# Kernel optimization log

Measured on AMD Instinct MI355X. Metric: run time of the kernel, lower is better.

Reference implementation:

```python
import jax, jax.numpy as jnp
import numpy as np

N, E, D = 50000, 640000, 128


def setup_inputs() -> dict:
    key = jax.random.key(0)
    ks = jax.random.split(key, 10)
    scale = (2.0 / (D + D)) ** 0.5  # xavier-ish scale for square weights

    def w(k):
        return jax.random.normal(k, (D, D), jnp.float32) * scale

    return {
        "x": jax.random.normal(ks[0], (N, D), jnp.float32),
        "view2": jax.random.normal(ks[1], (N, D), jnp.float32),
        "W_neigh1": w(ks[2]),
        "W_self1": w(ks[3]),
        "b_self1": jnp.zeros((D,), jnp.float32),
        "W_neigh2": w(ks[4]),
        "W_self2": w(ks[5]),
        "b_self2": jnp.zeros((D,), jnp.float32),
        "W_attn": w(ks[6]),
        "b_attn": jnp.zeros((D,), jnp.float32),
        "att": jax.random.normal(ks[7], (1, D), jnp.float32) * 0.1,
        "src": jax.random.randint(ks[8], (E,), 0, N),
        "dst": jax.random.randint(ks[9], (E,), 0, N),
    }


def _sage_mean(h, src, dst, W_neigh, W_self, b_self, n):
    """DGL SAGEConv, aggregator_type='mean', in_feats==out_feats (lin after mp)."""
    msgs = h[src]  # gather: [E, D]
    s = jax.ops.segment_sum(msgs, dst, num_segments=n)  # scatter-add: [N, D]
    deg = jax.ops.segment_sum(jnp.ones((src.shape[0],), h.dtype), dst, num_segments=n)
    h_neigh = jnp.where(deg[:, None] > 0, s / jnp.maximum(deg, 1.0)[:, None], 0.0)
    # rst = fc_self(h_self) + fc_neigh(h_neigh)
    return h @ W_self.T + b_self + h_neigh @ W_neigh.T


def reference(x, view2, W_neigh1, W_self1, b_self1, W_neigh2, W_self2, b_self2,
              W_attn, b_attn, att, src, dst):
    n = x.shape[0]
    # SAGENet: outs = [h, l1(h)/1, l2(l1(h))/2]; res = sum(outs)
    h1 = _sage_mean(x, src, dst, W_neigh1, W_self1, b_self1, n)
    h2 = _sage_mean(h1, src, dst, W_neigh2, W_self2, b_self2, n)
    res = x + h1 + h2 * 0.5
    # Attn semantic fusion over embedding views [res, view2]
    embeds = (res, view2)
    scores = jnp.stack(
        [att[0] @ jnp.tanh(e @ W_attn.T + b_attn).mean(axis=0) for e in embeds]
    )  # [2]
    beta = jax.nn.softmax(scores)
    return beta[0] * res + beta[1] * view2
```

## Files before the change

kernel.cpp:

```cpp
#include <hip/hip_runtime.h>

#define DD 128

using bf16 = __bf16;
typedef __bf16 bf16x8 __attribute__((ext_vector_type(8)));
typedef float f32x4 __attribute__((ext_vector_type(4)));

__device__ inline bf16x8 cvt8(const float* p) {
  f32x4 v0 = *(const f32x4*)p;
  f32x4 v1 = *(const f32x4*)(p + 4);
  bf16x8 r;
  r[0] = (bf16)v0[0]; r[1] = (bf16)v0[1]; r[2] = (bf16)v0[2]; r[3] = (bf16)v0[3];
  r[4] = (bf16)v1[0]; r[5] = (bf16)v1[1]; r[6] = (bf16)v1[2]; r[7] = (bf16)v1[3];
  return r;
}

__device__ inline float ftanh(float x) {
  float e2 = __expf(2.0f * x);
  return 1.0f - 2.0f * __builtin_amdgcn_rcpf(e2 + 1.0f);
}

__device__ inline int swz(int o) { return o ^ (((o >> 8) & 7) << 4); }

__global__ void k_prep(int* __restrict__ cnt, int N,
                       const float* __restrict__ w0, const float* __restrict__ w1,
                       const float* __restrict__ w2, const float* __restrict__ w3,
                       const float* __restrict__ w4, bf16* __restrict__ wb, int totalW,
                       const float* __restrict__ x, bf16* __restrict__ xb, int total8,
                       int nbZ, int nbW) {
  int b = blockIdx.x;
  if (b < nbZ) {
    int i = b * 256 + threadIdx.x;
    if (i < N) cnt[i] = 0;
  } else if (b < nbZ + nbW) {
    int i = (b - nbZ) * 256 + threadIdx.x;
    if (i < totalW) {
      int m = i >> 14;
      int r = i & 16383;
      const float* s = m == 0 ? w0 : m == 1 ? w1 : m == 2 ? w2 : m == 3 ? w3 : w4;
      wb[i] = (bf16)s[r];
    }
  } else {
    int i = (b - nbZ - nbW) * 256 + threadIdx.x;
    if (i < total8) *(bf16x8*)(xb + (size_t)i * 8) = cvt8(x + (size_t)i * 8);
  }
}

__global__ void k_hist(const int* __restrict__ dst, int* __restrict__ cnt, int E) {
  int e = blockIdx.x * 256 + threadIdx.x;
  if (e < E) atomicAdd(&cnt[dst[e]], 1);
}

__global__ __launch_bounds__(256) void k_scan1(const int* __restrict__ cnt,
                                               int* __restrict__ bsum, int N) {
  __shared__ int sm[256];
  int t = threadIdx.x;
  int i = blockIdx.x * 256 + t;
  sm[t] = (i < N) ? cnt[i] : 0;
  __syncthreads();
#pragma unroll
  for (int d = 128; d > 0; d >>= 1) {
    if (t < d) sm[t] += sm[t + d];
    __syncthreads();
  }
  if (t == 0) bsum[blockIdx.x] = sm[0];
}

__global__ __launch_bounds__(256) void k_scan2(int* __restrict__ bsum, int nb) {
  __shared__ int sm[256];
  int t = threadIdx.x;
  int v = (t < nb) ? bsum[t] : 0;
  sm[t] = v;
  __syncthreads();
#pragma unroll
  for (int d = 1; d < 256; d <<= 1) {
    int u = (t >= d) ? sm[t - d] : 0;
    __syncthreads();
    sm[t] += u;
    __syncthreads();
  }
  if (t < nb) bsum[t] = sm[t] - v;
}

__global__ __launch_bounds__(256) void k_scan3(const int* __restrict__ cnt,
                                               const int* __restrict__ bsum,
                                               int* __restrict__ offs,
                                               int* __restrict__ cursor, int N) {
  __shared__ int sm[256];
  int t = threadIdx.x;
  int i = blockIdx.x * 256 + t;
  int v = (i < N) ? cnt[i] : 0;
  sm[t] = v;
  __syncthreads();
#pragma unroll
  for (int d = 1; d < 256; d <<= 1) {
    int u = (t >= d) ? sm[t - d] : 0;
    __syncthreads();
    sm[t] += u;
    __syncthreads();
  }
  int incl = sm[t];
  int base = bsum[blockIdx.x];
  if (i < N) {
    int ex = base + incl - v;
    offs[i] = ex;
    cursor[i] = ex;
    if (i == N - 1) offs[N] = base + incl;
  }
}

__global__ void k_scatter(const int* __restrict__ src, const int* __restrict__ dst,
                          int* __restrict__ cursor, int* __restrict__ ssrc, int E) {
  int e = blockIdx.x * 256 + threadIdx.x;
  if (e < E) {
    int d = dst[e];
    int p = atomicAdd(&cursor[d], 1);
    ssrc[p] = src[e];
  }
}

template <int MODE>
__global__ __launch_bounds__(1024, 1) void k_layer(const bf16* __restrict__ Hb,
                                                   const int* __restrict__ offs,
                                                   const int* __restrict__ ssrc,
                                                   const bf16* __restrict__ Wsb,
                                                   const bf16* __restrict__ Wnb,
                                                   const float* __restrict__ bias,
                                                   const float* __restrict__ Xres,
                                                   bf16* __restrict__ H1out,
                                                   float* __restrict__ Out, int N) {
  __shared__ char smem[65536];
  int t = threadIdx.x;
#pragma unroll
  for (int m = 0; m < 2; ++m) {
    const bf16* wsrc = m ? Wnb : Wsb;
#pragma unroll
    for (int it = 0; it < 2; ++it) {
      int o = (it * 1024 + t) * 16;
      *(bf16x8*)(smem + m * 32768 + swz(o)) = *(const bf16x8*)(wsrc + o / 2);
    }
  }
  __syncthreads();

  int wv = t >> 6;
  int lane = t & 63;
  int tile = blockIdx.x * 16 + wv;
  int n0 = tile << 4;
  if (n0 >= N) return;
  int lr = lane & 15;
  int g = lane >> 4;
  int lk = g << 3;

  const bf16* a1p = Hb + (size_t)(n0 + lr) * DD + lk;
  bf16x8 a1[4];
#pragma unroll
  for (int kk = 0; kk < 4; ++kk) a1[kk] = *(const bf16x8*)(a1p + kk * 32);

  int node = n0 + lr;
  int beg = offs[node], end = offs[node + 1];
  float acc[4][8];
#pragma unroll
  for (int kk = 0; kk < 4; ++kk)
#pragma unroll
    for (int j = 0; j < 8; ++j) acc[kk][j] = 0.f;
  for (int i = beg; i < end; ++i) {
    int s = ssrc[i];
    const bf16* hp = Hb + (size_t)s * DD + lk;
#pragma unroll
    for (int kk = 0; kk < 4; ++kk) {
      bf16x8 v = *(const bf16x8*)(hp + kk * 32);
#pragma unroll
      for (int j = 0; j < 8; ++j) acc[kk][j] += (float)v[j];
    }
  }
  float inv = (end > beg) ? 1.0f / (float)(end - beg) : 0.f;
  bf16x8 a2[4];
#pragma unroll
  for (int kk = 0; kk < 4; ++kk)
#pragma unroll
    for (int j = 0; j < 8; ++j) a2[kk][j] = (bf16)(acc[kk][j] * inv);

  int rb = n0 + (g << 2);
#pragma unroll
  for (int j = 0; j < 8; ++j) {
    int row = j * 16 + lr;
    int rbase = row * 256 + lk * 2;
    f32x4 cs = {0.f, 0.f, 0.f, 0.f};
    f32x4 cn = {0.f, 0.f, 0.f, 0.f};
#pragma unroll
    for (int kk = 0; kk < 4; ++kk) {
      int ro = swz(rbase + kk * 64);
      bf16x8 bs = *(const bf16x8*)(smem + ro);
      bf16x8 bn = *(const bf16x8*)(smem + 32768 + ro);
      cs = __builtin_amdgcn_mfma_f32_16x16x32_bf16(a1[kk], bs, cs, 0, 0, 0);
      cn = __builtin_amdgcn_mfma_f32_16x16x32_bf16(a2[kk], bn, cn, 0, 0, 0);
    }
    int col = j * 16 + lr;
    float bb = bias[col];
#pragma unroll
    for (int r = 0; r < 4; ++r) {
      size_t idx = (size_t)(rb + r) * DD + col;
      float v = cs[r] + cn[r] + bb;
      if (MODE == 0) H1out[idx] = (bf16)v;
      else           Out[idx] = Xres[idx] + (float)Hb[idx] + 0.5f * v;
    }
  }
}

__global__ __launch_bounds__(512, 4) void k_attn2(const float* __restrict__ res,
                                                  const float* __restrict__ v2f,
                                                  const bf16* __restrict__ Wab,
                                                  const float* __restrict__ bias,
                                                  const float* __restrict__ att,
                                                  float* __restrict__ partial,
                                                  int nbA, int N) {
  __shared__ char smem[32768];
  __shared__ float smr[8];
  int t = threadIdx.x;
#pragma unroll
  for (int it = 0; it < 4; ++it) {
    int o = (it * 512 + t) * 16;
    *(bf16x8*)(smem + swz(o)) = *(const bf16x8*)(Wab + o / 2);
  }
  __syncthreads();

  int wv = t >> 6;
  int lane = t & 63;
  int gwid = blockIdx.x * 8 + wv;
  int view = gwid & 1;
  int tile = gwid >> 1;
  int n0 = tile << 4;
  float part = 0.f;
  if (n0 < N) {
    const float* Ef = view ? v2f : res;
    int lr = lane & 15;
    int lk = (lane >> 4) << 3;
    const float* ap = Ef + (size_t)(n0 + lr) * DD + lk;
    bf16x8 a[4];
#pragma unroll
    for (int kk = 0; kk < 4; ++kk) a[kk] = cvt8(ap + kk * 32);
#pragma unroll
    for (int j = 0; j < 8; ++j) {
      int row = j * 16 + lr;
      int rbase = row * 256 + lk * 2;
      f32x4 c = {0.f, 0.f, 0.f, 0.f};
#pragma unroll
      for (int kk = 0; kk < 4; ++kk) {
        bf16x8 bw = *(const bf16x8*)(smem + swz(rbase + kk * 64));
        c = __builtin_amdgcn_mfma_f32_16x16x32_bf16(a[kk], bw, c, 0, 0, 0);
      }
      int col = j * 16 + lr;
      float aw = att[col], bb = bias[col];
#pragma unroll
      for (int r = 0; r < 4; ++r) part += aw * ftanh(c[r] + bb);
    }
  }
#pragma unroll
  for (int d = 1; d < 64; d <<= 1) part += __shfl_xor(part, d);
  if (lane == 0) smr[wv] = part;
  __syncthreads();
  if (t == 0) {
    partial[blockIdx.x]       = smr[0] + smr[2] + smr[4] + smr[6];
    partial[nbA + blockIdx.x] = smr[1] + smr[3] + smr[5] + smr[7];
  }
}

__global__ __launch_bounds__(256) void k_score(const float* __restrict__ partial,
                                               float* __restrict__ scores, int nbA) {
  __shared__ float sm[256];
  int t = threadIdx.x;
#pragma unroll
  for (int v = 0; v < 2; ++v) {
    float s = 0.f;
    for (int i = t; i < nbA; i += 256) s += partial[v * nbA + i];
    sm[t] = s;
    __syncthreads();
#pragma unroll
    for (int d = 128; d > 0; d >>= 1) {
      if (t < d) sm[t] += sm[t + d];
      __syncthreads();
    }
    if (t == 0) scores[v] = sm[0];
    __syncthreads();
  }
}

__global__ void k_fin(float* out, const float* __restrict__ v2,
                      const float* __restrict__ scores, float invN, int total4) {
  int i = blockIdx.x * 256 + threadIdx.x;
  if (i >= total4) return;
  float s0 = scores[0] * invN, s1 = scores[1] * invN;
  float m = fmaxf(s0, s1);
  float e0 = expf(s0 - m), e1 = expf(s1 - m);
  float inv = 1.0f / (e0 + e1);
  float b0 = e0 * inv, b1 = e1 * inv;
  f32x4 r = ((const f32x4*)out)[i];
  f32x4 w = ((const f32x4*)v2)[i];
  f32x4 o;
  o[0] = b0 * r[0] + b1 * w[0];
  o[1] = b0 * r[1] + b1 * w[1];
  o[2] = b0 * r[2] + b1 * w[2];
  o[3] = b0 * r[3] + b1 * w[3];
  ((f32x4*)out)[i] = o;
}

extern "C" void kernel_launch(void* const* d_in, const int* in_sizes, int n_in,
                              void* d_out, int out_size, void* d_ws, size_t ws_size,
                              hipStream_t stream) {
  const float* x   = (const float*)d_in[0];
  const float* v2  = (const float*)d_in[1];
  const float* Wn1 = (const float*)d_in[2];
  const float* Ws1 = (const float*)d_in[3];
  const float* b1  = (const float*)d_in[4];
  const float* Wn2 = (const float*)d_in[5];
  const float* Ws2 = (const float*)d_in[6];
  const float* b2  = (const float*)d_in[7];
  const float* Wa  = (const float*)d_in[8];
  const float* ba  = (const float*)d_in[9];
  const float* att = (const float*)d_in[10];
  const int*  src  = (const int*)d_in[11];
  const int*  dst  = (const int*)d_in[12];
  const int D = in_sizes[4];
  const int N = in_sizes[0] / D;
  const int E = in_sizes[11];
  float* out = (float*)d_out;

  char* ws = (char*)d_ws;
  size_t o = 0;
  auto alloc = [&](size_t bytes) -> void* {
    void* p = ws + o;
    o += (bytes + 255) & ~(size_t)255;
    return p;
  };
  int*  cnt    = (int*)alloc((size_t)N * 4);
  int*  offs   = (int*)alloc((size_t)(N + 1) * 4);
  int*  cursor = (int*)alloc((size_t)N * 4);
  int*  ssrc   = (int*)alloc((size_t)E * 4);
  bf16* xb     = (bf16*)alloc((size_t)N * D * 2);
  bf16* h1b    = (bf16*)alloc((size_t)N * D * 2);
  bf16* wb     = (bf16*)alloc((size_t)5 * D * D * 2);
  float* sc    = (float*)alloc(2 * 4);
  int nb = (N + 255) / 256;
  int*  bsum   = (int*)alloc((size_t)nb * 4);

  int tilesPerView = (N + 15) / 16;
  int attnWaves = 2 * tilesPerView;
  int nbA = (attnWaves + 7) / 8;
  float* apart = (float*)alloc((size_t)2 * nbA * 4);

  int nbZ = (N + 255) / 256;
  int nbW = (5 * D * D + 255) / 256;
  int nbX = (N * D / 8 + 255) / 256;
  k_prep<<<nbZ + nbW + nbX, 256, 0, stream>>>(cnt, N, Ws1, Wn1, Ws2, Wn2, Wa, wb,
                                              5 * D * D, x, xb, N * D / 8, nbZ, nbW);

  k_hist<<<(E + 255) / 256, 256, 0, stream>>>(dst, cnt, E);
  k_scan1<<<nb, 256, 0, stream>>>(cnt, bsum, N);
  k_scan2<<<1, 256, 0, stream>>>(bsum, nb);
  k_scan3<<<nb, 256, 0, stream>>>(cnt, bsum, offs, cursor, N);
  k_scatter<<<(E + 255) / 256, 256, 0, stream>>>(src, dst, cursor, ssrc, E);

  int tiles = (N + 15) / 16;
  int layerBlocks = (tiles + 15) / 16;

  k_layer<0><<<layerBlocks, 1024, 0, stream>>>(xb, offs, ssrc, wb, wb + D * D, b1,
                                               nullptr, h1b, nullptr, N);
  k_layer<1><<<layerBlocks, 1024, 0, stream>>>(h1b, offs, ssrc, wb + 2 * D * D,
                                               wb + 3 * D * D, b2, x, nullptr, out, N);
  k_attn2<<<nbA, 512, 0, stream>>>(out, v2, wb + 4 * D * D, ba, att, apart, nbA, N);
  k_score<<<1, 256, 0, stream>>>(apart, sc, nbA);
  k_fin<<<((N * D / 4) + 255) / 256, 256, 0, stream>>>(out, v2, sc, 1.0f / (float)N, N * D / 4);
}
```

Measured before the change: 195.5 us.

## Sort nodes by in-degree for layer load balance and store residual as bf16

Builds a node permutation sorted by in-degree (descending, capped at 63) using a small histogram, scan and atomic placement. The layer kernels process nodes in that order, so each 16-node wave holds nodes of similar degree and lanes spend less time idle on imbalanced gather loops. The residual output is now kept as a bf16 buffer that feeds the attention and final kernels, cutting fp32 read and write traffic. The cost is three extra small launches and scattered output writes. The bf16 residual also lowers the precision of the final output.

```diff
diff --git a/kernel.cpp b/kernel.cpp
--- a/kernel.cpp
+++ b/kernel.cpp
@@ -22,13 +22,14 @@
 
 __device__ inline int swz(int o) { return o ^ (((o >> 8) & 7) << 4); }
 
-__global__ void k_prep(int* __restrict__ cnt, int N,
+__global__ void k_prep(int* __restrict__ cnt, int* __restrict__ dbin, int N,
                        const float* __restrict__ w0, const float* __restrict__ w1,
                        const float* __restrict__ w2, const float* __restrict__ w3,
                        const float* __restrict__ w4, bf16* __restrict__ wb, int totalW,
                        const float* __restrict__ x, bf16* __restrict__ xb, int total8,
                        int nbZ, int nbW) {
   int b = blockIdx.x;
+  if (b == 0 && threadIdx.x < 64) dbin[threadIdx.x] = 0;
   if (b < nbZ) {
     int i = b * 256 + threadIdx.x;
     if (i < N) cnt[i] = 0;
@@ -119,16 +120,39 @@
   }
 }
 
+__global__ void k_dhist(const int* __restrict__ cnt, int* __restrict__ dbin, int N) {
+  int i = blockIdx.x * 256 + threadIdx.x;
+  if (i < N) atomicAdd(&dbin[min(cnt[i], 63)], 1);
+}
+
+__global__ void k_dscan(const int* __restrict__ dbin, int* __restrict__ dcur) {
+  int t = threadIdx.x;
+  int s = 0;
+  for (int b = t + 1; b < 64; ++b) s += dbin[b];
+  dcur[t] = s;
+}
+
+__global__ void k_dperm(const int* __restrict__ cnt, int* __restrict__ dcur,
+                        int* __restrict__ perm, int N) {
+  int i = blockIdx.x * 256 + threadIdx.x;
+  if (i < N) {
+    int b = min(cnt[i], 63);
+    int p = atomicAdd(&dcur[b], 1);
+    perm[p] = i;
+  }
+}
+
 template <int MODE>
 __global__ __launch_bounds__(1024, 1) void k_layer(const bf16* __restrict__ Hb,
                                                    const int* __restrict__ offs,
                                                    const int* __restrict__ ssrc,
+                                                   const int* __restrict__ perm,
                                                    const bf16* __restrict__ Wsb,
                                                    const bf16* __restrict__ Wnb,
                                                    const float* __restrict__ bias,
                                                    const float* __restrict__ Xres,
                                                    bf16* __restrict__ H1out,
-                                                   float* __restrict__ Out, int N) {
+                                                   bf16* __restrict__ Resb, int N) {
   __shared__ char smem[65536];
   int t = threadIdx.x;
 #pragma unroll
@@ -151,12 +175,13 @@
   int g = lane >> 4;
   int lk = g << 3;
 
-  const bf16* a1p = Hb + (size_t)(n0 + lr) * DD + lk;
+  int node = perm[n0 + lr];
+
+  const bf16* a1p = Hb + (size_t)node * DD + lk;
   bf16x8 a1[4];
 #pragma unroll
   for (int kk = 0; kk < 4; ++kk) a1[kk] = *(const bf16x8*)(a1p + kk * 32);
 
-  int node = n0 + lr;
   int beg = offs[node], end = offs[node + 1];
   float acc[4][8];
 #pragma unroll
@@ -180,7 +205,9 @@
 #pragma unroll
     for (int j = 0; j < 8; ++j) a2[kk][j] = (bf16)(acc[kk][j] * inv);
 
-  int rb = n0 + (g << 2);
+  const int4 p4 = *(const int4*)(perm + n0 + (g << 2));
+  const int* prow = (const int*)&p4;
+
 #pragma unroll
   for (int j = 0; j < 8; ++j) {
     int row = j * 16 + lr;
@@ -199,15 +226,15 @@
     float bb = bias[col];
 #pragma unroll
     for (int r = 0; r < 4; ++r) {
-      size_t idx = (size_t)(rb + r) * DD + col;
+      size_t idx = (size_t)prow[r] * DD + col;
       float v = cs[r] + cn[r] + bb;
       if (MODE == 0) H1out[idx] = (bf16)v;
-      else           Out[idx] = Xres[idx] + (float)Hb[idx] + 0.5f * v;
-    }
-  }
-}
-
-__global__ __launch_bounds__(512, 4) void k_attn2(const float* __restrict__ res,
+      else           Resb[idx] = (bf16)(Xres[idx] + (float)Hb[idx] + 0.5f * v);
+    }
+  }
+}
+
+__global__ __launch_bounds__(512, 4) void k_attn2(const bf16* __restrict__ resb,
                                                   const float* __restrict__ v2f,
                                                   const bf16* __restrict__ Wab,
                                                   const float* __restrict__ bias,
@@ -232,13 +259,18 @@
   int n0 = tile << 4;
   float part = 0.f;
   if (n0 < N) {
-    const float* Ef = view ? v2f : res;
     int lr = lane & 15;
     int lk = (lane >> 4) << 3;
-    const float* ap = Ef + (size_t)(n0 + lr) * DD + lk;
     bf16x8 a[4];
-#pragma unroll
-    for (int kk = 0; kk < 4; ++kk) a[kk] = cvt8(ap + kk * 32);
+    if (view) {
+      const float* ap = v2f + (size_t)(n0 + lr) * DD + lk;
+#pragma unroll
+      for (int kk = 0; kk < 4; ++kk) a[kk] = cvt8(ap + kk * 32);
+    } else {
+      const bf16* ap = resb + (size_t)(n0 + lr) * DD + lk;
+#pragma unroll
+      for (int kk = 0; kk < 4; ++kk) a[kk] = *(const bf16x8*)(ap + kk * 32);
+    }
 #pragma unroll
     for (int j = 0; j < 8; ++j) {
       int row = j * 16 + lr;
@@ -285,23 +317,27 @@
   }
 }
 
-__global__ void k_fin(float* out, const float* __restrict__ v2,
-                      const float* __restrict__ scores, float invN, int total4) {
+__global__ void k_fin(float* __restrict__ out, const bf16* __restrict__ resb,
+                      const float* __restrict__ v2,
+                      const float* __restrict__ scores, float invN, int total8) {
   int i = blockIdx.x * 256 + threadIdx.x;
-  if (i >= total4) return;
+  if (i >= total8) return;
   float s0 = scores[0] * invN, s1 = scores[1] * invN;
   float m = fmaxf(s0, s1);
   float e0 = expf(s0 - m), e1 = expf(s1 - m);
   float inv = 1.0f / (e0 + e1);
   float b0 = e0 * inv, b1 = e1 * inv;
-  f32x4 r = ((const f32x4*)out)[i];
-  f32x4 w = ((const f32x4*)v2)[i];
-  f32x4 o;
-  o[0] = b0 * r[0] + b1 * w[0];
-  o[1] = b0 * r[1] + b1 * w[1];
-  o[2] = b0 * r[2] + b1 * w[2];
-  o[3] = b0 * r[3] + b1 * w[3];
-  ((f32x4*)out)[i] = o;
+  bf16x8 r = ((const bf16x8*)resb)[i];
+  f32x4 w0 = ((const f32x4*)v2)[2 * i];
+  f32x4 w1 = ((const f32x4*)v2)[2 * i + 1];
+  f32x4 o0, o1;
+#pragma unroll
+  for (int j = 0; j < 4; ++j) {
+    o0[j] = b0 * (float)r[j] + b1 * w0[j];
+    o1[j] = b0 * (float)r[4 + j] + b1 * w1[j];
+  }
+  ((f32x4*)out)[2 * i] = o0;
+  ((f32x4*)out)[2 * i + 1] = o1;
 }
 
 extern "C" void kernel_launch(void* const* d_in, const int* in_sizes, int n_in,
@@ -336,8 +372,12 @@
   int*  offs   = (int*)alloc((size_t)(N + 1) * 4);
   int*  cursor = (int*)alloc((size_t)N * 4);
   int*  ssrc   = (int*)alloc((size_t)E * 4);
+  int*  perm   = (int*)alloc((size_t)N * 4);
+  int*  dbin   = (int*)alloc(64 * 4);
+  int*  dcur   = (int*)alloc(64 * 4);
   bf16* xb     = (bf16*)alloc((size_t)N * D * 2);
   bf16* h1b    = (bf16*)alloc((size_t)N * D * 2);
+  bf16* resb   = (bf16*)alloc((size_t)N * D * 2);
   bf16* wb     = (bf16*)alloc((size_t)5 * D * D * 2);
   float* sc    = (float*)alloc(2 * 4);
   int nb = (N + 255) / 256;
@@ -351,23 +391,27 @@
   int nbZ = (N + 255) / 256;
   int nbW = (5 * D * D + 255) / 256;
   int nbX = (N * D / 8 + 255) / 256;
-  k_prep<<<nbZ + nbW + nbX, 256, 0, stream>>>(cnt, N, Ws1, Wn1, Ws2, Wn2, Wa, wb,
+  k_prep<<<nbZ + nbW + nbX, 256, 0, stream>>>(cnt, dbin, N, Ws1, Wn1, Ws2, Wn2, Wa, wb,
                                               5 * D * D, x, xb, N * D / 8, nbZ, nbW);
 
   k_hist<<<(E + 255) / 256, 256, 0, stream>>>(dst, cnt, E);
   k_scan1<<<nb, 256, 0, stream>>>(cnt, bsum, N);
   k_scan2<<<1, 256, 0, stream>>>(bsum, nb);
   k_scan3<<<nb, 256, 0, stream>>>(cnt, bsum, offs, cursor, N);
+  k_dhist<<<nb, 256, 0, stream>>>(cnt, dbin, N);
+  k_dscan<<<1, 64, 0, stream>>>(dbin, dcur);
+  k_dperm<<<nb, 256, 0, stream>>>(cnt, dcur, perm, N);
   k_scatter<<<(E + 255) / 256, 256, 0, stream>>>(src, dst, cursor, ssrc, E);
 
   int tiles = (N + 15) / 16;
   int layerBlocks = (tiles + 15) / 16;
 
-  k_layer<0><<<layerBlocks, 1024, 0, stream>>>(xb, offs, ssrc, wb, wb + D * D, b1,
-                                               nullptr, h1b, nullptr, N);
-  k_layer<1><<<layerBlocks, 1024, 0, stream>>>(h1b, offs, ssrc, wb + 2 * D * D,
-                                               wb + 3 * D * D, b2, x, nullptr, out, N);
-  k_attn2<<<nbA, 512, 0, stream>>>(out, v2, wb + 4 * D * D, ba, att, apart, nbA, N);
+  k_layer<0><<<layerBlocks, 1024, 0, stream>>>(xb, offs, ssrc, perm, wb, wb + D * D,
+                                               b1, nullptr, h1b, nullptr, N);
+  k_layer<1><<<layerBlocks, 1024, 0, stream>>>(h1b, offs, ssrc, perm, wb + 2 * D * D,
+                                               wb + 3 * D * D, b2, x, nullptr, resb, N);
+  k_attn2<<<nbA, 512, 0, stream>>>(resb, v2, wb + 4 * D * D, ba, att, apart, nbA, N);
   k_score<<<1, 256, 0, stream>>>(apart, sc, nbA);
-  k_fin<<<((N * D / 4) + 255) / 256, 256, 0, stream>>>(out, v2, sc, 1.0f / (float)N, N * D / 4);
-}
+  k_fin<<<((N * D / 8) + 255) / 256, 256, 0, stream>>>(out, resb, v2, sc,
+                                                       1.0f / (float)N, N * D / 8);
+}
```

After: 534.5 us. 173% more time.
